# Kernel optimization log

Hardware: AMD Instinct MI355X
Metric: run time of the kernel (lower is better)

Reference implementation:

```python
import jax, jax.numpy as jnp
import numpy as np
from jax import lax

VOCAB, ENC_DIM, PRED_H, JOINT_H = 4096, 1024, 640, 640
T, MAX_SYM, BLANK, SOS = 128, 30, 0, -1
S = T * (MAX_SYM + 1)  # upper bound on greedy-decode loop iterations


def setup_inputs() -> dict:
    key = jax.random.key(0)
    ks = jax.random.split(key, 10)
    rn = lambda k, shape, s: jax.random.normal(k, shape, jnp.float32) * s
    return {
        "enc_out": rn(ks[0], (1, T, ENC_DIM), 1.0),
        "out_len": T,
        "emb": rn(ks[1], (VOCAB, PRED_H), 0.1),
        "Wih0": rn(ks[2], (4 * PRED_H, PRED_H), 0.04),
        "Whh0": rn(ks[3], (4 * PRED_H, PRED_H), 0.04),
        "b0": jnp.zeros((4 * PRED_H,), jnp.float32),
        "Wih1": rn(ks[4], (4 * PRED_H, PRED_H), 0.04),
        "Whh1": rn(ks[5], (4 * PRED_H, PRED_H), 0.04),
        "b1": jnp.zeros((4 * PRED_H,), jnp.float32),
        "Wj1": rn(ks[6], (JOINT_H, ENC_DIM + PRED_H), 0.03),
        "bj1": jnp.zeros((JOINT_H,), jnp.float32),
        "Wj2": rn(ks[7], (VOCAB, JOINT_H), 0.04),
        "bj2": jnp.zeros((VOCAB,), jnp.float32),
    }


def _lstm_cell(x, h, c, Wih, Whh, b):
    z = x @ Wih.T + h @ Whh.T + b  # [4H], torch gate order i,f,g,o
    i, f, g, o = jnp.split(z, 4)
    c2 = jax.nn.sigmoid(f) * c + jax.nn.sigmoid(i) * jnp.tanh(g)
    return jax.nn.sigmoid(o) * jnp.tanh(c2), c2


def _decode(enc_out, timesteps, emb, Wih0, Whh0, b0, Wih1, Whh1, b1, Wj1, bj1, Wj2, bj2):
    enc = enc_out[0]  # [T, ENC_DIM]

    def step(carry, _):
        t, sa, last, h0, c0, h1, c1, labels, cnt, done = carry
        # prediction net step (SOS = -1 -> zero embedding)
        g_in = jnp.where(last < 0, 0.0, emb[jnp.maximum(last, 0)])
        h0n, c0n = _lstm_cell(g_in, h0, c0, Wih0, Whh0, b0)
        h1n, c1n = _lstm_cell(h0n, h1, c1, Wih1, Whh1, b1)
        # joint net on current encoder frame
        f = enc[jnp.minimum(t, T - 1)]
        hid = jax.nn.relu(Wj1 @ jnp.concatenate([f, h1n]) + bj1)
        logits = Wj2 @ hid + bj2  # [VOCAB]
        k = jnp.argmax(logits).astype(jnp.int32)
        stop_sym = (k == BLANK) | (sa >= MAX_SYM)
        emit = (~stop_sym) & (~done)
        adv = stop_sym & (~done)
        # emit: append symbol, keep hidden'; blank/max: advance time, discard hidden'
        last2 = jnp.where(emit, k, last)
        h0 = jnp.where(emit, h0n, h0); c0 = jnp.where(emit, c0n, c0)
        h1 = jnp.where(emit, h1n, h1); c1 = jnp.where(emit, c1n, c1)
        labels = labels.at[cnt].set(jnp.where(emit, k, labels[cnt]))
        cnt2 = cnt + emit.astype(jnp.int32)
        sa2 = jnp.where(emit, sa + 1, jnp.where(adv, 0, sa))
        t2 = t + adv.astype(jnp.int32)
        done2 = done | (adv & (t2 >= timesteps))
        out_logits = jnp.where(done, 0.0, logits)
        return (t2, sa2, last2, h0, c0, h1, c1, labels, cnt2, done2), out_logits

    zeros = jnp.zeros((PRED_H,), jnp.float32)
    carry0 = (jnp.int32(0), jnp.int32(0), jnp.int32(SOS),
              zeros, zeros, zeros, zeros,
              jnp.full((S,), -1, jnp.int32), jnp.int32(0), jnp.bool_(False))
    carry, logits_seq = lax.scan(step, carry0, None, length=S)
    labels, cnt = carry[7], carry[8]
    return logits_seq, labels, cnt


def reference(enc_out, out_len, emb, Wih0, Whh0, b0, Wih1, Whh1, b1, Wj1, bj1, Wj2, bj2):
    return _decode(enc_out, out_len, emb, Wih0, Whh0, b0, Wih1, Whh1, b1, Wj1, bj1, Wj2, bj2)
```

## Files before the change

kernel.cpp:

```cpp
#include <hip/hip_runtime.h>
#include <cmath>

#define VOCAB   4096
#define ENC_DIM 1024
#define PRED_H  640
#define JOINT_H 640
#define TMAX    128
#define MAX_SYM 30
#define NSTEPS  (TMAX*(MAX_SYM+1))
#define NWG     160
#define NTHR    512
#define RLX __ATOMIC_RELAXED
#define AGT __HIP_MEMORY_SCOPE_AGENT

typedef unsigned long long u64;
typedef __attribute__((ext_vector_type(4))) unsigned int u32x4;


__device__ __forceinline__ float wave_red(float v){
  v += __shfl_xor(v, 32, 64);
  v += __shfl_xor(v, 16, 64);
  v += __shfl_xor(v,  8, 64);
  v += __shfl_xor(v,  4, 64);
  v += __shfl_xor(v,  2, 64);
  v += __shfl_xor(v,  1, 64);
  return v;
}

__device__ __forceinline__ float sigf(float x){ return 1.0f/(1.0f+expf(-x)); }

__device__ __forceinline__ void tstore(u64* p, float v, unsigned tag){
  __hip_atomic_store(p, ((u64)tag<<32) | (u64)__float_as_uint(v), RLX, AGT);
}

__device__ __forceinline__ u32x4 cload_u4(const u64* p){
  u32x4 r;
  asm volatile("global_load_dwordx4 %0, %1, off sc0 sc1" : "=v"(r) : "v"(p));
  return r;
}

__device__ __forceinline__ void pollchunk(u64* src, float* dst, unsigned tag, int c){
  u64* p = src + (c<<1);
  u32x4 v;
  for(;;){
    v = cload_u4(p);
    asm volatile("s_waitcnt vmcnt(0)" ::: "memory");
    if (v.y == tag && v.w == tag) break;
    __builtin_amdgcn_s_sleep(8);
  }
  __builtin_amdgcn_sched_barrier(0);
  dst[(c<<1)]   = __uint_as_float(v.x);
  dst[(c<<1)+1] = __uint_as_float(v.z);
}

__device__ __forceinline__ u64 mkentry(float lg, int r, unsigned ep){
  unsigned u = __float_as_uint(lg);
  u = (u & 0x80000000u) ? ~u : (u | 0x80000000u);
  return ((u64)u<<24) | ((u64)(ep&0xFFFu)<<12) | (u64)(4095 - r);
}

__global__ void init_ws(unsigned* ws){
  for (int i = threadIdx.x; i < 8192; i += 256) ws[i] = 0u;
}

__global__ __launch_bounds__(NTHR, 2)
void rnnt_decode(const float* __restrict__ enc,
                 const int*   __restrict__ outlen_p,
                 const float* __restrict__ emb,
                 const float* __restrict__ Wih0, const float* __restrict__ Whh0, const float* __restrict__ b0,
                 const float* __restrict__ Wih1, const float* __restrict__ Whh1, const float* __restrict__ b1,
                 const float* __restrict__ Wj1,  const float* __restrict__ bj1,
                 const float* __restrict__ Wj2,  const float* __restrict__ bj2,
                 float* __restrict__ out,
                 u64* __restrict__ parts,
                 u64* __restrict__ bufsT,
                 u64* __restrict__ hidT)
{
  const int wg = blockIdx.x, tid = threadIdx.x;
  const int wave = tid >> 6, lane = tid & 63;
  const int timesteps = outlen_p[0];

  __shared__ float xa[PRED_H];
  __shared__ float xsh[ENC_DIM];
  __shared__ float h0buf[2][PRED_H];
  __shared__ float h1buf[2][PRED_H];
  __shared__ float hidsh[JOINT_H];
  __shared__ float zsh[4][4];
  __shared__ float zjsA[8], zjsB[8];
  __shared__ float c0c[4], c1c[4], c0p[4], c1p[4];
  __shared__ float bj1sh[4];
  __shared__ u64 psh[8];
  __shared__ u64 pmx[3];
  __shared__ int kshm;

  const int jb = wg*4;

  const int gA = wave & 3;
  const int jA = wave >> 2;
  const int rowA = gA*PRED_H + jb + jA;
  const int rowB = gA*PRED_H + jb + jA + 2;

  float w0xA[10], w0hA[10], w0xB[10], w0hB[10];
  float w1xA[10], w1hA[10], w1xB[10], w1hB[10];
  #pragma unroll
  for (int i = 0; i < 10; ++i){
    int c = lane + (i<<6);
    w0xA[i] = Wih0[(size_t)rowA*PRED_H + c];
    w0hA[i] = Whh0[(size_t)rowA*PRED_H + c];
    w1xA[i] = Wih1[(size_t)rowA*PRED_H + c];
    w1hA[i] = Whh1[(size_t)rowA*PRED_H + c];
    w0xB[i] = Wih0[(size_t)rowB*PRED_H + c];
    w0hB[i] = Whh0[(size_t)rowB*PRED_H + c];
    w1xB[i] = Wih1[(size_t)rowB*PRED_H + c];
    w1hB[i] = Whh1[(size_t)rowB*PRED_H + c];
  }
  const float bA0 = b0[rowA], bA1 = b1[rowA];
  const float bB0 = b0[rowB], bB1 = b1[rowB];

  const int grp = wave >> 2;
  const int vt  = ((wave & 3)<<6) | lane;
  const int rP0 = jb + grp;
  const int rP1 = jb + 2 + grp;
  float wjf0[4], wjh0[3], wjf1[4], wjh1[3];
  #pragma unroll
  for (int i = 0; i < 4; ++i){
    wjf0[i] = Wj1[(size_t)rP0*(ENC_DIM+PRED_H) + vt + (i<<8)];
    wjf1[i] = Wj1[(size_t)rP1*(ENC_DIM+PRED_H) + vt + (i<<8)];
  }
  #pragma unroll
  for (int i = 0; i < 3; ++i){
    int c = vt + (i<<8);
    wjh0[i] = (c < PRED_H) ? Wj1[(size_t)rP0*(ENC_DIM+PRED_H) + ENC_DIM + c] : 0.f;
    wjh1[i] = (c < PRED_H) ? Wj1[(size_t)rP1*(ENC_DIM+PRED_H) + ENC_DIM + c] : 0.f;
  }
  float ca0 = 0.f, ca1 = 0.f;

  const int nrows = (wg < 96) ? 26 : 25;
  const int r2b = wg*25 + (wg < 96 ? wg : 96);
  float wj2[4][10], bj2r[4];
  #pragma unroll
  for (int p = 0; p < 4; ++p){
    bool act = (p*8 + wave) < nrows;
    int r = act ? (r2b + p*8 + wave) : 0;
    #pragma unroll
    for (int i = 0; i < 10; ++i)
      wj2[p][i] = act ? Wj2[(size_t)r*JOINT_H + lane + (i<<6)] : 0.f;
    bj2r[p] = act ? bj2[r] : 0.f;
  }

  for (int i = tid; i < PRED_H; i += NTHR){ h0buf[0][i] = 0.f; h1buf[0][i] = 0.f; }
  if (tid < 4){ c0c[tid] = 0.f; c1c[tid] = 0.f; bj1sh[tid] = bj1[jb+tid]; }
  __syncthreads();

  int cur = 0, t = 0, sa = 0, last = -1, cnt = 0, tStaged = -1;
  bool done = false, reuse = false;

  for (int s = 0; s < NSTEPS; ++s){
    if (done){
      if (wg < 8) out[(size_t)s*VOCAB + wg*NTHR + tid] = 0.f;
      continue;
    }
    const unsigned tag = (unsigned)(s + 1);

    if (!reuse){
      for (int i = tid; i < PRED_H; i += NTHR)
        xa[i] = (last >= 0) ? emb[(size_t)last*PRED_H + i] : 0.f;
      __syncthreads();
      {
        float acc = 0.f;
        #pragma unroll
        for (int i = 0; i < 10; ++i) acc = fmaf(w0xA[i], xa[lane+(i<<6)], acc);
        #pragma unroll
        for (int i = 0; i < 10; ++i) acc = fmaf(w0hA[i], h0buf[cur][lane+(i<<6)], acc);
        acc = wave_red(acc);
        if (lane == 0) zsh[gA][jA] = acc + bA0;
        float a2 = 0.f;
        #pragma unroll
        for (int i = 0; i < 10; ++i) a2 = fmaf(w0xB[i], xa[lane+(i<<6)], a2);
        #pragma unroll
        for (int i = 0; i < 10; ++i) a2 = fmaf(w0hB[i], h0buf[cur][lane+(i<<6)], a2);
        a2 = wave_red(a2);
        if (lane == 0) zsh[gA][jA+2] = a2 + bB0;
      }
      __syncthreads();
      if (tid < 4){
        float ig = sigf(zsh[0][tid]), fg = sigf(zsh[1][tid]);
        float gg = tanhf(zsh[2][tid]), og = sigf(zsh[3][tid]);
        float c2 = fg*c0c[tid] + ig*gg;
        c0p[tid] = c2;
        tstore(&bufsT[jb+tid], og*tanhf(c2), tag);
      }
      __syncthreads();

      if (tid < 320) pollchunk(bufsT, h0buf[cur^1], tag, tid);
      __syncthreads();
      {
        float acc = 0.f;
        #pragma unroll
        for (int i = 0; i < 10; ++i) acc = fmaf(w1xA[i], h0buf[cur^1][lane+(i<<6)], acc);
        #pragma unroll
        for (int i = 0; i < 10; ++i) acc = fmaf(w1hA[i], h1buf[cur][lane+(i<<6)], acc);
        acc = wave_red(acc);
        if (lane == 0) zsh[gA][jA] = acc + bA1;
        float a2 = 0.f;
        #pragma unroll
        for (int i = 0; i < 10; ++i) a2 = fmaf(w1xB[i], h0buf[cur^1][lane+(i<<6)], a2);
        #pragma unroll
        for (int i = 0; i < 10; ++i) a2 = fmaf(w1hB[i], h1buf[cur][lane+(i<<6)], a2);
        a2 = wave_red(a2);
        if (lane == 0) zsh[gA][jA+2] = a2 + bB1;
      }
      __syncthreads();
      if (tid < 4){
        float ig = sigf(zsh[0][tid]), fg = sigf(zsh[1][tid]);
        float gg = tanhf(zsh[2][tid]), og = sigf(zsh[3][tid]);
        float c2 = fg*c1c[tid] + ig*gg;
        c1p[tid] = c2;
        tstore(&bufsT[PRED_H+jb+tid], og*tanhf(c2), tag);
      }
    }

    {
      int tcap = (t < TMAX-1) ? t : (TMAX-1);
      bool fNew = (tcap != tStaged);
      if (fNew)
        for (int i = tid; i < ENC_DIM; i += NTHR) xsh[i] = enc[(size_t)tcap*ENC_DIM + i];
      if (!reuse){
        if (tid < 320) pollchunk(bufsT + PRED_H, h1buf[cur^1], tag, tid);
      }
      __syncthreads();
      if (fNew){
        float a = 0.f, b = 0.f;
        #pragma unroll
        for (int i = 0; i < 4; ++i){
          a = fmaf(wjf0[i], xsh[vt+(i<<8)], a);
          b = fmaf(wjf1[i], xsh[vt+(i<<8)], b);
        }
        ca0 = a; ca1 = b;
        tStaged = tcap;
      }
      {
        float acc = ca0;
        #pragma unroll
        for (int i = 0; i < 3; ++i){
          int c = vt + (i<<8);
          acc = fmaf(wjh0[i], h1buf[cur^1][(c < PRED_H) ? c : 0], acc);
        }
        acc = wave_red(acc);
        if (lane == 0) zjsA[wave] = acc;
        float acc2 = ca1;
        #pragma unroll
        for (int i = 0; i < 3; ++i){
          int c = vt + (i<<8);
          acc2 = fmaf(wjh1[i], h1buf[cur^1][(c < PRED_H) ? c : 0], acc2);
        }
        acc2 = wave_red(acc2);
        if (lane == 0) zjsB[wave] = acc2;
      }
      __syncthreads();
      if (tid == 0){
        float v0 = zjsA[0]+zjsA[1]+zjsA[2]+zjsA[3] + bj1sh[0];
        tstore(&hidT[jb],   v0 > 0.f ? v0 : 0.f, tag);
        float v1 = zjsA[4]+zjsA[5]+zjsA[6]+zjsA[7] + bj1sh[1];
        tstore(&hidT[jb+1], v1 > 0.f ? v1 : 0.f, tag);
        float v2 = zjsB[0]+zjsB[1]+zjsB[2]+zjsB[3] + bj1sh[2];
        tstore(&hidT[jb+2], v2 > 0.f ? v2 : 0.f, tag);
        float v3 = zjsB[4]+zjsB[5]+zjsB[6]+zjsB[7] + bj1sh[3];
        tstore(&hidT[jb+3], v3 > 0.f ? v3 : 0.f, tag);
      }
    }

    int k;
    {
      if (tid < 320) pollchunk(hidT, hidsh, tag, tid);
      __syncthreads();
      u64 best = 0;
      #pragma unroll
      for (int p = 0; p < 4; ++p){
        if (p*8 + wave < nrows){
          int r = r2b + p*8 + wave;
          float acc = 0.f;
          #pragma unroll
          for (int i = 0; i < 10; ++i) acc = fmaf(wj2[p][i], hidsh[lane+(i<<6)], acc);
          acc = wave_red(acc);
          if (lane == 0){
            float lg = acc + bj2r[p];
            out[(size_t)s*VOCAB + r] = lg;
            u64 e = mkentry(lg, r, tag);
            if (e > best) best = e;
          }
        }
      }
      if (lane == 0) psh[wave] = best;
      __syncthreads();
      if (tid == 0){
        u64 m = psh[0];
        #pragma unroll
        for (int w = 1; w < 8; ++w) if (psh[w] > m) m = psh[w];
        __hip_atomic_store(&parts[wg], m, RLX, AGT);
      }
      u64 myp = 0;
      if (tid < 160){
        for(;;){
          u64 e = __hip_atomic_load(&parts[tid], RLX, AGT);
          if ((unsigned)((e>>12) & 0xFFFu) == (tag & 0xFFFu)){ myp = e; break; }
          __builtin_amdgcn_s_sleep(4);
        }
      }
      if (wave < 3){
        #pragma unroll
        for (int off = 32; off; off >>= 1){
          u64 o = __shfl_xor(myp, off, 64);
          if (o > myp) myp = o;
        }
        if (lane == 0) pmx[wave] = myp;
      }
      __syncthreads();
      u64 m = pmx[0];
      if (pmx[1] > m) m = pmx[1];
      if (pmx[2] > m) m = pmx[2];
      k = 4095 - (int)(m & 0xFFFull);
    }

    bool stop = (k == 0) || (sa >= MAX_SYM);
    if (!stop){
      if (wg == 0 && tid == 0) out[(size_t)NSTEPS*VOCAB + cnt] = (float)k;
      if (tid < 4){ c0c[tid] = c0p[tid]; c1c[tid] = c1p[tid]; }
      cnt++; sa++; last = k; cur ^= 1; reuse = false;
    } else {
      sa = 0; t++; reuse = true;
      if (t >= timesteps) done = true;
    }
    __syncthreads();
  }

  size_t lab = (size_t)NSTEPS*VOCAB;
  int gidx = wg*NTHR + tid;
  for (int i = cnt + gidx; i < NSTEPS; i += NWG*NTHR) out[lab + i] = -1.f;
  if (wg == 0 && tid == 0) out[lab + NSTEPS] = (float)cnt;
}

extern "C" void kernel_launch(void* const* d_in, const int* in_sizes, int n_in,
                              void* d_out, int out_size, void* d_ws, size_t ws_size,
                              hipStream_t stream) {
  const float* enc  = (const float*)d_in[0];
  const int*   olen = (const int*)  d_in[1];
  const float* emb  = (const float*)d_in[2];
  const float* Wih0 = (const float*)d_in[3];
  const float* Whh0 = (const float*)d_in[4];
  const float* b0   = (const float*)d_in[5];
  const float* Wih1 = (const float*)d_in[6];
  const float* Whh1 = (const float*)d_in[7];
  const float* b1   = (const float*)d_in[8];
  const float* Wj1  = (const float*)d_in[9];
  const float* bj1  = (const float*)d_in[10];
  const float* Wj2  = (const float*)d_in[11];
  const float* bj2  = (const float*)d_in[12];
  float* out = (float*)d_out;

  u64* parts = (u64*)d_ws;
  u64* bufsT = (u64*)((char*)d_ws + 4096);
  u64* hidT  = (u64*)((char*)d_ws + 14336);

  init_ws<<<1, 256, 0, stream>>>((unsigned*)d_ws);

  void* args[] = {&enc,&olen,&emb,&Wih0,&Whh0,&b0,&Wih1,&Whh1,&b1,
                  &Wj1,&bj1,&Wj2,&bj2,&out,&parts,&bufsT,&hidT};
  hipLaunchCooperativeKernel((const void*)rnnt_decode, dim3(NWG), dim3(NTHR),
                             args, 0, stream);
}
```

Baseline: 50.33 ms.

## Replace tagged-value polling with flag+data handoff per workgroup, padded slots

Cross-workgroup exchange of h0/h1/hidden values now uses one 16-byte data slot plus a separate flag per workgroup, on its own 64-byte slot. Previously each value carried its own tag in a 64-bit word and 320 threads polled. Now only 160 threads poll a single flag each, then read a vec4 of data. The partial-argmax slots are padded to separate cache lines and the sleep intervals are shortened. This trades an extra dependent load and a store fence per hop for fewer polled words and less false sharing.

```diff
diff --git a/kernel.cpp b/kernel.cpp
--- a/kernel.cpp
+++ b/kernel.cpp
@@ -14,7 +14,7 @@
 #define AGT __HIP_MEMORY_SCOPE_AGENT
 
 typedef unsigned long long u64;
-typedef __attribute__((ext_vector_type(4))) unsigned int u32x4;
+typedef __attribute__((ext_vector_type(4))) float f32x4;
 
 
 __device__ __forceinline__ float wave_red(float v){
@@ -29,28 +29,29 @@
 
 __device__ __forceinline__ float sigf(float x){ return 1.0f/(1.0f+expf(-x)); }
 
-__device__ __forceinline__ void tstore(u64* p, float v, unsigned tag){
-  __hip_atomic_store(p, ((u64)tag<<32) | (u64)__float_as_uint(v), RLX, AGT);
-}
-
-__device__ __forceinline__ u32x4 cload_u4(const u64* p){
-  u32x4 r;
-  asm volatile("global_load_dwordx4 %0, %1, off sc0 sc1" : "=v"(r) : "v"(p));
-  return r;
-}
-
-__device__ __forceinline__ void pollchunk(u64* src, float* dst, unsigned tag, int c){
-  u64* p = src + (c<<1);
-  u32x4 v;
+__device__ __forceinline__ void hop_send(float* data, unsigned* flag, int w,
+                                         f32x4 v, unsigned tag){
+  asm volatile("global_store_dwordx4 %0, %1, off sc0 sc1"
+               :: "v"(data + (w<<4)), "v"(v) : "memory");
+  asm volatile("s_waitcnt vmcnt(0)" ::: "memory");
+  __hip_atomic_store(flag + (w<<4), tag, RLX, AGT);
+}
+
+__device__ __forceinline__ void hop_recv(const unsigned* flag, const float* data,
+                                         float* dstLDS, unsigned tag, int i){
+  const unsigned* fp = flag + (i<<4);
   for(;;){
-    v = cload_u4(p);
-    asm volatile("s_waitcnt vmcnt(0)" ::: "memory");
-    if (v.y == tag && v.w == tag) break;
-    __builtin_amdgcn_s_sleep(8);
-  }
+    unsigned f;
+    asm volatile("global_load_dword %0, %1, off sc0 sc1\n\ts_waitcnt vmcnt(0)"
+                 : "=v"(f) : "v"(fp) : "memory");
+    if (f >= tag) break;
+    __builtin_amdgcn_s_sleep(2);
+  }
+  f32x4 v;
+  asm volatile("global_load_dwordx4 %0, %1, off sc0 sc1\n\ts_waitcnt vmcnt(0)"
+               : "=v"(v) : "v"(data + (i<<4)) : "memory");
   __builtin_amdgcn_sched_barrier(0);
-  dst[(c<<1)]   = __uint_as_float(v.x);
-  dst[(c<<1)+1] = __uint_as_float(v.z);
+  *(f32x4*)&dstLDS[i<<2] = v;
 }
 
 __device__ __forceinline__ u64 mkentry(float lg, int r, unsigned ep){
@@ -60,7 +61,7 @@
 }
 
 __global__ void init_ws(unsigned* ws){
-  for (int i = threadIdx.x; i < 8192; i += 256) ws[i] = 0u;
+  for (int i = threadIdx.x; i < 18432; i += 256) ws[i] = 0u;
 }
 
 __global__ __launch_bounds__(NTHR, 2)
@@ -72,13 +73,19 @@
                  const float* __restrict__ Wj1,  const float* __restrict__ bj1,
                  const float* __restrict__ Wj2,  const float* __restrict__ bj2,
                  float* __restrict__ out,
-                 u64* __restrict__ parts,
-                 u64* __restrict__ bufsT,
-                 u64* __restrict__ hidT)
+                 char* __restrict__ ws)
 {
   const int wg = blockIdx.x, tid = threadIdx.x;
   const int wave = tid >> 6, lane = tid & 63;
   const int timesteps = outlen_p[0];
+
+  unsigned* flagA = (unsigned*)(ws);
+  unsigned* flagB = (unsigned*)(ws + 10240);
+  unsigned* flagH = (unsigned*)(ws + 20480);
+  float*    dataA = (float*)   (ws + 30720);
+  float*    dataB = (float*)   (ws + 40960);
+  float*    dataH = (float*)   (ws + 51200);
+  u64*      parts = (u64*)     (ws + 61440);
 
   __shared__ float xa[PRED_H];
   __shared__ float xsh[ENC_DIM];
@@ -91,7 +98,6 @@
   __shared__ float bj1sh[4];
   __shared__ u64 psh[8];
   __shared__ u64 pmx[3];
-  __shared__ int kshm;
 
   const int jb = wg*4;
 
@@ -183,16 +189,22 @@
         if (lane == 0) zsh[gA][jA+2] = a2 + bB0;
       }
       __syncthreads();
-      if (tid < 4){
-        float ig = sigf(zsh[0][tid]), fg = sigf(zsh[1][tid]);
-        float gg = tanhf(zsh[2][tid]), og = sigf(zsh[3][tid]);
-        float c2 = fg*c0c[tid] + ig*gg;
-        c0p[tid] = c2;
-        tstore(&bufsT[jb+tid], og*tanhf(c2), tag);
-      }
-      __syncthreads();
-
-      if (tid < 320) pollchunk(bufsT, h0buf[cur^1], tag, tid);
+      if (wave == 0){
+        float hv = 0.f;
+        if (lane < 4){
+          float ig = sigf(zsh[0][lane]), fg = sigf(zsh[1][lane]);
+          float gg = tanhf(zsh[2][lane]), og = sigf(zsh[3][lane]);
+          float c2 = fg*c0c[lane] + ig*gg;
+          c0p[lane] = c2;
+          hv = og*tanhf(c2);
+        }
+        f32x4 v;
+        v.x = __shfl(hv, 0, 64); v.y = __shfl(hv, 1, 64);
+        v.z = __shfl(hv, 2, 64); v.w = __shfl(hv, 3, 64);
+        if (lane == 0) hop_send(dataA, flagA, wg, v, tag);
+      }
+
+      if (tid < 160) hop_recv(flagA, dataA, h0buf[cur^1], tag, tid);
       __syncthreads();
       {
         float acc = 0.f;
@@ -211,12 +223,19 @@
         if (lane == 0) zsh[gA][jA+2] = a2 + bB1;
       }
       __syncthreads();
-      if (tid < 4){
-        float ig = sigf(zsh[0][tid]), fg = sigf(zsh[1][tid]);
-        float gg = tanhf(zsh[2][tid]), og = sigf(zsh[3][tid]);
-        float c2 = fg*c1c[tid] + ig*gg;
-        c1p[tid] = c2;
-        tstore(&bufsT[PRED_H+jb+tid], og*tanhf(c2), tag);
+      if (wave == 0){
+        float hv = 0.f;
+        if (lane < 4){
+          float ig = sigf(zsh[0][lane]), fg = sigf(zsh[1][lane]);
+          float gg = tanhf(zsh[2][lane]), og = sigf(zsh[3][lane]);
+          float c2 = fg*c1c[lane] + ig*gg;
+          c1p[lane] = c2;
+          hv = og*tanhf(c2);
+        }
+        f32x4 v;
+        v.x = __shfl(hv, 0, 64); v.y = __shfl(hv, 1, 64);
+        v.z = __shfl(hv, 2, 64); v.w = __shfl(hv, 3, 64);
+        if (lane == 0) hop_send(dataB, flagB, wg, v, tag);
       }
     }
 
@@ -226,7 +245,7 @@
       if (fNew)
         for (int i = tid; i < ENC_DIM; i += NTHR) xsh[i] = enc[(size_t)tcap*ENC_DIM + i];
       if (!reuse){
-        if (tid < 320) pollchunk(bufsT + PRED_H, h1buf[cur^1], tag, tid);
+        if (tid < 160) hop_recv(flagB, dataB, h1buf[cur^1], tag, tid);
       }
       __syncthreads();
       if (fNew){
@@ -258,21 +277,26 @@
         if (lane == 0) zjsB[wave] = acc2;
       }
       __syncthreads();
-      if (tid == 0){
-        float v0 = zjsA[0]+zjsA[1]+zjsA[2]+zjsA[3] + bj1sh[0];
-        tstore(&hidT[jb],   v0 > 0.f ? v0 : 0.f, tag);
-        float v1 = zjsA[4]+zjsA[5]+zjsA[6]+zjsA[7] + bj1sh[1];
-        tstore(&hidT[jb+1], v1 > 0.f ? v1 : 0.f, tag);
-        float v2 = zjsB[0]+zjsB[1]+zjsB[2]+zjsB[3] + bj1sh[2];
-        tstore(&hidT[jb+2], v2 > 0.f ? v2 : 0.f, tag);
-        float v3 = zjsB[4]+zjsB[5]+zjsB[6]+zjsB[7] + bj1sh[3];
-        tstore(&hidT[jb+3], v3 > 0.f ? v3 : 0.f, tag);
+      if (wave == 0){
+        float hv = 0.f;
+        if (lane < 4){
+          float v;
+          if (lane == 0)      v = zjsA[0]+zjsA[1]+zjsA[2]+zjsA[3] + bj1sh[0];
+          else if (lane == 1) v = zjsA[4]+zjsA[5]+zjsA[6]+zjsA[7] + bj1sh[1];
+          else if (lane == 2) v = zjsB[0]+zjsB[1]+zjsB[2]+zjsB[3] + bj1sh[2];
+          else                v = zjsB[4]+zjsB[5]+zjsB[6]+zjsB[7] + bj1sh[3];
+          hv = v > 0.f ? v : 0.f;
+        }
+        f32x4 v;
+        v.x = __shfl(hv, 0, 64); v.y = __shfl(hv, 1, 64);
+        v.z = __shfl(hv, 2, 64); v.w = __shfl(hv, 3, 64);
+        if (lane == 0) hop_send(dataH, flagH, wg, v, tag);
       }
     }
 
     int k;
     {
-      if (tid < 320) pollchunk(hidT, hidsh, tag, tid);
+      if (tid < 160) hop_recv(flagH, dataH, hidsh, tag, tid);
       __syncthreads();
       u64 best = 0;
       #pragma unroll
@@ -297,14 +321,14 @@
         u64 m = psh[0];
         #pragma unroll
         for (int w = 1; w < 8; ++w) if (psh[w] > m) m = psh[w];
-        __hip_atomic_store(&parts[wg], m, RLX, AGT);
+        __hip_atomic_store(&parts[(size_t)wg<<3], m, RLX, AGT);
       }
       u64 myp = 0;
       if (tid < 160){
         for(;;){
-          u64 e = __hip_atomic_load(&parts[tid], RLX, AGT);
+          u64 e = __hip_atomic_load(&parts[(size_t)tid<<3], RLX, AGT);
           if ((unsigned)((e>>12) & 0xFFFu) == (tag & 0xFFFu)){ myp = e; break; }
-          __builtin_amdgcn_s_sleep(4);
+          __builtin_amdgcn_s_sleep(2);
         }
       }
       if (wave < 3){
@@ -357,15 +381,12 @@
   const float* Wj2  = (const float*)d_in[11];
   const float* bj2  = (const float*)d_in[12];
   float* out = (float*)d_out;
-
-  u64* parts = (u64*)d_ws;
-  u64* bufsT = (u64*)((char*)d_ws + 4096);
-  u64* hidT  = (u64*)((char*)d_ws + 14336);
+  char* ws = (char*)d_ws;
 
   init_ws<<<1, 256, 0, stream>>>((unsigned*)d_ws);
 
   void* args[] = {&enc,&olen,&emb,&Wih0,&Whh0,&b0,&Wih1,&Whh1,&b1,
-                  &Wj1,&bj1,&Wj2,&bj2,&out,&parts,&bufsT,&hidT};
+                  &Wj1,&bj1,&Wj2,&bj2,&out,&ws};
   hipLaunchCooperativeKernel((const void*)rnnt_decode, dim3(NWG), dim3(NTHR),
                              args, 0, stream);
 }
```

New measurement: 47.38 ms. -5.8%, faster.
